# Kernel tuning notes

Hardware: AMD Instinct MI355X
Metric: run time of the kernel (lower is better)

Reference implementation:

```python
import jax, jax.numpy as jnp
import numpy as np

EXP_EMBD = 1024
EXP_Q_H = 8
EXP_HEAD_DIM = 256
EXP_KV_H = 1
EXP_KV_DIM = EXP_KV_H * EXP_HEAD_DIM  # 256
EXP_FFN = 4096
B, L, LC = 8, 512, 2048


def setup_inputs() -> dict:
    key = jax.random.key(0)
    ks = jax.random.split(key, 12)
    def w(k, shape):
        fan_in = shape[-1]
        return jax.random.normal(k, shape, jnp.float32) * (fan_in ** -0.5)
    return {
        "x": jax.random.normal(ks[0], (B, L, EXP_EMBD), jnp.float32),
        "text_k": jax.random.normal(ks[1], (B, LC, EXP_KV_DIM), jnp.float32),
        "text_v": jax.random.normal(ks[2], (B, LC, EXP_KV_DIM), jnp.float32),
        "ln1_w": jnp.ones((EXP_EMBD,), jnp.float32),
        "ln2_w": jnp.ones((EXP_EMBD,), jnp.float32),
        "Wq": w(ks[3], (EXP_Q_H * EXP_HEAD_DIM, EXP_EMBD)),
        "Wk": w(ks[4], (EXP_KV_DIM, EXP_KV_DIM)),
        "Wv": w(ks[5], (EXP_KV_DIM, EXP_KV_DIM)),
        "Wo": w(ks[6], (EXP_EMBD, EXP_Q_H * EXP_HEAD_DIM)),
        "Wg": w(ks[7], (EXP_FFN, EXP_EMBD)),
        "Wu": w(ks[8], (EXP_FFN, EXP_EMBD)),
        "Wd": w(ks[9], (EXP_EMBD, EXP_FFN)),
    }


def _rmsnorm(x, w):
    # torch.nn.RMSNorm with eps=None -> eps = finfo(dtype).eps
    eps = jnp.asarray(jnp.finfo(jnp.float32).eps, x.dtype)
    return x * jax.lax.rsqrt(jnp.mean(x * x, axis=-1, keepdims=True) + eps) * w


def _rope(x):
    # x: [B, L, H, D]
    b, l, h, d = x.shape
    d2 = d // 2
    ts = 10000.0 ** (2.0 / d * jnp.arange(d2, dtype=jnp.float32))  # [d2]
    rad = jnp.arange(l, dtype=jnp.float32)[:, None] / ts[None, :]  # [L, d2]
    s = jnp.sin(rad)[None, :, None, :]
    c = jnp.cos(rad)[None, :, None, :]
    x1, x2 = x[..., :d2], x[..., d2:]
    return jnp.concatenate([x1 * c - x2 * s, x2 * c + x1 * s], axis=-1)


def reference(x, text_k, text_v, ln1_w, ln2_w, Wq, Wk, Wv, Wo, Wg, Wu, Wd):
    b, l, _ = x.shape
    lc = text_k.shape[1]
    residual = x
    h = _rmsnorm(x, ln1_w)
    q = _rope((h @ Wq.T).reshape(b, l, EXP_Q_H, EXP_HEAD_DIM))          # [B,L,QH,D]
    k = (text_k @ Wk.T).reshape(b, lc, EXP_KV_H, EXP_HEAD_DIM)          # [B,Lc,KVH,D]
    v = (text_v @ Wv.T).reshape(b, lc, EXP_KV_H, EXP_HEAD_DIM)
    kv_map = (jnp.arange(EXP_Q_H) * EXP_KV_H) // EXP_Q_H                # GQA head map
    kh = jnp.take(k, kv_map, axis=2)                                    # [B,Lc,QH,D]
    vh = jnp.take(v, kv_map, axis=2)
    scale = 1.0 / np.sqrt(EXP_HEAD_DIM).astype(np.float32)
    scores = jnp.einsum('blhd,bchd->bhlc', q, kh) * scale               # [B,QH,L,Lc]
    attn = jax.nn.softmax(scores, axis=-1)
    ctx = jnp.einsum('bhlc,bchd->blhd', attn, vh).reshape(b, l, -1)
    x = ctx @ Wo.T + residual
    residual = x
    h = _rmsnorm(x, ln2_w)
    return (jax.nn.silu(h @ Wg.T) * (h @ Wu.T)) @ Wd.T + residual
```

## Files before the change

kernel.cpp:

```cpp
#include <hip/hip_runtime.h>

typedef __attribute__((ext_vector_type(4))) float f32x4;
typedef __attribute__((ext_vector_type(8))) short s16x8;
typedef __attribute__((ext_vector_type(4))) unsigned short u16x4;

#define B_    8
#define L_    512
#define LC_   2048
#define EMBD  1024

__device__ __forceinline__ float b2f(unsigned short u) {
  unsigned int i = ((unsigned int)u) << 16;
  float f; __builtin_memcpy(&f, &i, 4); return f;
}
__device__ __forceinline__ unsigned short f2b(float f) {
  unsigned int i; __builtin_memcpy(&i, &f, 4);
  unsigned int r = i + 0x7FFFu + ((i >> 16) & 1u);
  return (unsigned short)(r >> 16);
}

#define GLL16(g, l)                                                         \
  __builtin_amdgcn_global_load_lds(                                         \
      (__attribute__((address_space(1))) void*)(g),                         \
      (__attribute__((address_space(3))) void*)(l), 16, 0, 0)

#define VMCNT6() asm volatile("s_waitcnt vmcnt(6)" ::: "memory")
#define VMCNT0() asm volatile("s_waitcnt vmcnt(0)" ::: "memory")
#define LGKM0()  asm volatile("s_waitcnt lgkmcnt(0)" ::: "memory")

__global__ __launch_bounds__(256) void convert_f32_bf16(
    const float* __restrict__ in, unsigned short* __restrict__ out, int n4) {
  int i = blockIdx.x * 256 + threadIdx.x;
  if (i >= n4) return;
  float4 v = ((const float4*)in)[i];
  u16x4 o = { f2b(v.x), f2b(v.y), f2b(v.z), f2b(v.w) };
  ((u16x4*)out)[i] = o;
}

__global__ __launch_bounds__(256) void rmsnorm_kernel(
    const float* __restrict__ x, const float* __restrict__ w,
    unsigned short* __restrict__ out) {
  int row = blockIdx.x;
  int tid = threadIdx.x;
  float4 v = ((const float4*)(x + (size_t)row * EMBD))[tid];
  float ss = v.x*v.x + v.y*v.y + v.z*v.z + v.w*v.w;
#pragma unroll
  for (int o = 1; o < 64; o <<= 1) ss += __shfl_xor(ss, o);
  __shared__ float red[4];
  if ((tid & 63) == 0) red[tid >> 6] = ss;
  __syncthreads();
  float tot = red[0] + red[1] + red[2] + red[3];
  float rs = rsqrtf(tot * (1.0f / EMBD) + 1.1920928955078125e-07f);
  float4 wv = ((const float4*)w)[tid];
  u16x4 o = { f2b(v.x*rs*wv.x), f2b(v.y*rs*wv.y), f2b(v.z*rs*wv.z), f2b(v.w*rs*wv.w) };
  ((u16x4*)(out + (size_t)row * EMBD))[tid] = o;
}

__global__ __launch_bounds__(256) void rope_kernel(unsigned short* __restrict__ q) {
  int idx = blockIdx.x * 256 + threadIdx.x;
  int i   = idx & 127;
  int h   = (idx >> 7) & 7;
  int row = idx >> 10;
  int l   = row & (L_ - 1);
  size_t base = (size_t)row * 2048 + h * 256 + i;
  float x1 = b2f(q[base]);
  float x2 = b2f(q[base + 128]);
  float ts  = powf(10000.0f, (float)i * (2.0f / 256.0f));
  float rad = (float)l / ts;
  float s, c;
  sincosf(rad, &s, &c);
  q[base]       = f2b(x1 * c - x2 * s);
  q[base + 128] = f2b(x2 * c + x1 * s);
}

__global__ __launch_bounds__(256) void act_kernel(
    const unsigned short* __restrict__ g, const unsigned short* __restrict__ u,
    unsigned short* __restrict__ out, int n8) {
  int i = blockIdx.x * 256 + threadIdx.x;
  if (i >= n8) return;
  s16x8 gv = ((const s16x8*)g)[i];
  s16x8 uv = ((const s16x8*)u)[i];
  s16x8 ov;
#pragma unroll
  for (int j = 0; j < 8; ++j) {
    float gf = b2f((unsigned short)gv[j]);
    float uf = b2f((unsigned short)uv[j]);
    float s  = gf / (1.0f + __expf(-gf));
    ov[j] = (short)f2b(s * uf);
  }
  ((s16x8*)out)[i] = ov;
}

template <int ADD_RES, int OUT_BF16>
__global__ __launch_bounds__(256, 2) void gemm_nt(
    const unsigned short* __restrict__ A, const unsigned short* __restrict__ Bw,
    const float* __restrict__ Res, void* __restrict__ C, int M, int N, int K) {
  __shared__ unsigned short As[128 * 64];
  __shared__ unsigned short Bs[128 * 64];
  const int tid = threadIdx.x;
  const int lane = tid & 63, wid = tid >> 6;
  const int l15 = lane & 15, l4 = lane >> 4;
  const int wr = wid >> 1, wc = wid & 1;
  const int m0 = blockIdx.y * 128, n0 = blockIdx.x * 128;

  const f32x4 fz = {0.f, 0.f, 0.f, 0.f};
  f32x4 acc[4][4];
#pragma unroll
  for (int i = 0; i < 4; ++i)
#pragma unroll
    for (int j = 0; j < 4; ++j) acc[i][j] = fz;

  for (int k0 = 0; k0 < K; k0 += 64) {
    __syncthreads();
#pragma unroll
    for (int i = 0; i < 4; ++i) {
      int Li = i * 4096 + tid * 16;
      int row = Li >> 7;
      int kb = (Li & 127) ^ ((row & 7) << 4);
      GLL16((const char*)(A + (size_t)(m0 + row) * K + k0) + kb, (char*)As + Li);
      GLL16((const char*)(Bw + (size_t)(n0 + row) * K + k0) + kb, (char*)Bs + Li);
    }
    __syncthreads();
#pragma unroll
    for (int kk = 0; kk < 2; ++kk) {
      s16x8 af[4], bfr[4];
#pragma unroll
      for (int mi = 0; mi < 4; ++mi) {
        int row = wr * 64 + mi * 16 + l15;
        int kb = (kk * 64 + l4 * 16) ^ ((row & 7) << 4);
        af[mi] = *(const s16x8*)((const char*)As + row * 128 + kb);
      }
#pragma unroll
      for (int ni = 0; ni < 4; ++ni) {
        int row = wc * 64 + ni * 16 + l15;
        int kb = (kk * 64 + l4 * 16) ^ ((row & 7) << 4);
        bfr[ni] = *(const s16x8*)((const char*)Bs + row * 128 + kb);
      }
#pragma unroll
      for (int mi = 0; mi < 4; ++mi)
#pragma unroll
        for (int ni = 0; ni < 4; ++ni)
          acc[mi][ni] = __builtin_amdgcn_mfma_f32_16x16x32_bf16(
              af[mi], bfr[ni], acc[mi][ni], 0, 0, 0);
    }
  }
#pragma unroll
  for (int mi = 0; mi < 4; ++mi) {
#pragma unroll
    for (int r = 0; r < 4; ++r) {
      int grow = m0 + wr * 64 + mi * 16 + l4 * 4 + r;
      size_t base = (size_t)grow * N + n0 + wc * 64 + l15;
#pragma unroll
      for (int ni = 0; ni < 4; ++ni) {
        float v = acc[mi][ni][r];
        size_t idx = base + ni * 16;
        if (ADD_RES) v += Res[idx];
        if (OUT_BF16) ((unsigned short*)C)[idx] = f2b(v);
        else          ((float*)C)[idx] = v;
      }
    }
  }
}

__global__ __launch_bounds__(512, 2) void gemm256(
    const unsigned short* __restrict__ A, const unsigned short* __restrict__ Bw,
    unsigned short* __restrict__ C, int M, int N, int K) {
  extern __shared__ char smem[];
  const int tid = threadIdx.x;
  const int lane = tid & 63;
  const int wid = tid >> 6;
  const int wr = wid >> 2, wc = wid & 3;
  const int l15 = lane & 15, g = lane >> 4;
  int flat = blockIdx.y * 16 + blockIdx.x;
  flat = (flat & 7) * 32 + (flat >> 3);
  const int m0 = (flat >> 4) * 256, n0 = (flat & 15) * 256;
  const int T = K >> 6;
  const int swz = (l15 & 7) << 4;

  auto stage = [&](int t, int mat, int half) {
    char* dst = smem + mat * 65536 + (t & 1) * 32768 + half * 16384;
    const unsigned short* src = (mat ? Bw + (size_t)(n0 + half * 128) * K
                                     : A + (size_t)(m0 + half * 128) * K) + t * 64;
#pragma unroll
    for (int i = 0; i < 2; ++i) {
      int Li = i * 8192 + tid * 16;
      int row = Li >> 7;
      int kb = (Li & 127) ^ ((row & 7) << 4);
      GLL16((const char*)(src + (size_t)row * K) + kb, dst + Li);
    }
  };

  const f32x4 fz = {0.f, 0.f, 0.f, 0.f};
  f32x4 acc[2][2][4][2];
#pragma unroll
  for (int ms = 0; ms < 2; ++ms)
#pragma unroll
    for (int ns = 0; ns < 2; ++ns)
#pragma unroll
      for (int mi = 0; mi < 4; ++mi)
#pragma unroll
        for (int ni = 0; ni < 2; ++ni) acc[ms][ns][mi][ni] = fz;

  stage(0, 1, 0); stage(0, 1, 1); stage(0, 0, 0); stage(0, 0, 1);
  stage(1, 1, 0); stage(1, 1, 1); stage(1, 0, 0);
  VMCNT6();
  __builtin_amdgcn_s_barrier();

  for (int t = 0; t < T; ++t) {
    char* Ab = smem + (t & 1) * 32768 + wr * 16384;
    char* Bb = smem + 65536 + (t & 1) * 32768 + (wc >> 1) * 16384;
    const int bn = (wc & 1) * 64;
    s16x8 a[4][2], b0[2][2], b1[2][2];

#pragma unroll
    for (int mi = 0; mi < 4; ++mi) {
      int row = mi * 16 + l15;
#pragma unroll
      for (int kk = 0; kk < 2; ++kk)
        a[mi][kk] = *(const s16x8*)(Ab + row * 128 + ((kk * 64 + g * 16) ^ swz));
    }
#pragma unroll
    for (int ni = 0; ni < 2; ++ni) {
      int r0 = (bn + ni * 16 + l15) * 128;
      int r1 = (bn + 32 + ni * 16 + l15) * 128;
#pragma unroll
      for (int kk = 0; kk < 2; ++kk) {
        int ko = (kk * 64 + g * 16) ^ swz;
        b0[ni][kk] = *(const s16x8*)(Bb + r0 + ko);
        b1[ni][kk] = *(const s16x8*)(Bb + r1 + ko);
      }
    }
    if (t + 1 < T) stage(t + 1, 0, 1);
    __builtin_amdgcn_s_barrier();
    LGKM0();
    __builtin_amdgcn_sched_barrier(0);
    __builtin_amdgcn_s_setprio(1);
#pragma unroll
    for (int mi = 0; mi < 4; ++mi)
#pragma unroll
      for (int ni = 0; ni < 2; ++ni)
#pragma unroll
        for (int kk = 0; kk < 2; ++kk)
          acc[0][0][mi][ni] = __builtin_amdgcn_mfma_f32_16x16x32_bf16(
              a[mi][kk], b0[ni][kk], acc[0][0][mi][ni], 0, 0, 0);
    __builtin_amdgcn_s_setprio(0);
    __builtin_amdgcn_s_barrier();

    if (t + 2 < T) stage(t + 2, 1, 0);
    __builtin_amdgcn_s_barrier();
    __builtin_amdgcn_s_setprio(1);
#pragma unroll
    for (int mi = 0; mi < 4; ++mi)
#pragma unroll
      for (int ni = 0; ni < 2; ++ni)
#pragma unroll
        for (int kk = 0; kk < 2; ++kk)
          acc[0][1][mi][ni] = __builtin_amdgcn_mfma_f32_16x16x32_bf16(
              a[mi][kk], b1[ni][kk], acc[0][1][mi][ni], 0, 0, 0);
    __builtin_amdgcn_s_setprio(0);
    __builtin_amdgcn_s_barrier();

#pragma unroll
    for (int mi = 0; mi < 4; ++mi) {
      int row = 64 + mi * 16 + l15;
#pragma unroll
      for (int kk = 0; kk < 2; ++kk)
        a[mi][kk] = *(const s16x8*)(Ab + row * 128 + ((kk * 64 + g * 16) ^ swz));
    }
    if (t + 2 < T) stage(t + 2, 1, 1);
    __builtin_amdgcn_s_barrier();
    LGKM0();
    __builtin_amdgcn_sched_barrier(0);
    __builtin_amdgcn_s_setprio(1);
#pragma unroll
    for (int mi = 0; mi < 4; ++mi)
#pragma unroll
      for (int ni = 0; ni < 2; ++ni)
#pragma unroll
        for (int kk = 0; kk < 2; ++kk)
          acc[1][0][mi][ni] = __builtin_amdgcn_mfma_f32_16x16x32_bf16(
              a[mi][kk], b0[ni][kk], acc[1][0][mi][ni], 0, 0, 0);
    __builtin_amdgcn_s_setprio(0);
    __builtin_amdgcn_s_barrier();

    if (t + 2 < T) { stage(t + 2, 0, 0); VMCNT6(); }
    else           { VMCNT0(); }
    __builtin_amdgcn_s_barrier();
    __builtin_amdgcn_s_setprio(1);
#pragma unroll
    for (int mi = 0; mi < 4; ++mi)
#pragma unroll
      for (int ni = 0; ni < 2; ++ni)
#pragma unroll
        for (int kk = 0; kk < 2; ++kk)
          acc[1][1][mi][ni] = __builtin_amdgcn_mfma_f32_16x16x32_bf16(
              a[mi][kk], b1[ni][kk], acc[1][1][mi][ni], 0, 0, 0);
    __builtin_amdgcn_s_setprio(0);
    __builtin_amdgcn_s_barrier();
  }

#pragma unroll
  for (int ms = 0; ms < 2; ++ms)
#pragma unroll
    for (int mi = 0; mi < 4; ++mi)
#pragma unroll
      for (int r = 0; r < 4; ++r) {
        int grow = m0 + wr * 128 + ms * 64 + mi * 16 + g * 4 + r;
        size_t base = (size_t)grow * N + n0 + wc * 64;
#pragma unroll
        for (int ns = 0; ns < 2; ++ns)
#pragma unroll
          for (int ni = 0; ni < 2; ++ni)
            C[base + ns * 32 + ni * 16 + l15] = f2b(acc[ms][ns][mi][ni][r]);
      }
}

#define SWZV(d) (((((d) & 7) ^ (((d) >> 3) & 7))) << 4)

__global__ __launch_bounds__(512, 2) void attn_kernel(
    const unsigned short* __restrict__ Q,
    const unsigned short* __restrict__ Kc,
    const unsigned short* __restrict__ Vc,
    unsigned short* __restrict__ Ctx) {
  __shared__ unsigned short Ks[64 * 256];
  __shared__ unsigned short Vt[256 * 64];
  const int tid = threadIdx.x;
  const int lane = tid & 63, wid = tid >> 6;
  const int l15 = lane & 15, g = lane >> 4;
  const int qt = blockIdx.x, h = blockIdx.y, b = blockIdx.z;

  const size_t qrow = (size_t)(b * L_ + qt * 128 + wid * 16 + l15);
  const unsigned short* qp = Q + qrow * 2048 + h * 256;
  s16x8 qf[8];
#pragma unroll
  for (int kc = 0; kc < 8; ++kc) qf[kc] = *(const s16x8*)(qp + kc * 32 + g * 8);

  const f32x4 fz = {0.f, 0.f, 0.f, 0.f};
  f32x4 oacc[16];
#pragma unroll
  for (int i = 0; i < 16; ++i) oacc[i] = fz;
  float m_run = -__builtin_inff(), l_run = 0.f;

  const unsigned short* Kb = Kc + (size_t)b * LC_ * 256;
  const unsigned short* Vb = Vc + (size_t)b * LC_ * 256;

  for (int kt = 0; kt < LC_ / 64; ++kt) {
    __syncthreads();
#pragma unroll
    for (int i = 0; i < 4; ++i) {
      int Li = i * 8192 + tid * 16;
      int row = Li >> 9;
      int kb = (Li & 511) ^ ((row & 7) << 4);
      GLL16((const char*)(Kb + (size_t)(kt * 64 + row) * 256) + kb, (char*)Ks + Li);
    }
#pragma unroll
    for (int p = 0; p < 2; ++p) {
      int id = p * 512 + tid;
      int dgrp = id & 31;
      int kvp = id >> 5;
      int d0 = dgrp * 8, kv0 = kvp * 2;
      const unsigned short* v0p = Vb + (size_t)(kt * 64 + kv0) * 256 + d0;
      s16x8 r0 = *(const s16x8*)v0p;
      s16x8 r1 = *(const s16x8*)(v0p + 256);
#pragma unroll
      for (int j = 0; j < 8; ++j) {
        int d = d0 + j;
        unsigned int val = (unsigned int)(unsigned short)r0[j] |
                           ((unsigned int)(unsigned short)r1[j] << 16);
        *(unsigned int*)((char*)Vt + d * 128 + ((kv0 * 2) ^ SWZV(d))) = val;
      }
    }
    __syncthreads();

    f32x4 sacc[4];
#pragma unroll
    for (int mi = 0; mi < 4; ++mi) sacc[mi] = fz;
#pragma unroll
    for (int mi = 0; mi < 4; ++mi) {
      int row = mi * 16 + l15;
      int swz = (row & 7) << 4;
#pragma unroll
      for (int kc = 0; kc < 8; ++kc) {
        s16x8 kf = *(const s16x8*)((const char*)Ks + row * 512 + ((kc * 64 + g * 16) ^ swz));
        sacc[mi] = __builtin_amdgcn_mfma_f32_16x16x32_bf16(kf, qf[kc], sacc[mi], 0, 0, 0);
      }
    }
    float sv[4][4];
    float mt = -__builtin_inff();
#pragma unroll
    for (int mi = 0; mi < 4; ++mi)
#pragma unroll
      for (int r = 0; r < 4; ++r) {
        float t = sacc[mi][r] * 0.0625f;
        sv[mi][r] = t;
        mt = fmaxf(mt, t);
      }
    mt = fmaxf(mt, __shfl_xor(mt, 16));
    mt = fmaxf(mt, __shfl_xor(mt, 32));
    float mnew = fmaxf(m_run, mt);
    float alpha = __expf(m_run - mnew);
    float rs = 0.f;
#pragma unroll
    for (int mi = 0; mi < 4; ++mi)
#pragma unroll
      for (int r = 0; r < 4; ++r) {
        float p = __expf(sv[mi][r] - mnew);
        sv[mi][r] = p;
        rs += p;
      }
    rs += __shfl_xor(rs, 16);
    rs += __shfl_xor(rs, 32);
    l_run = l_run * alpha + rs;
    m_run = mnew;
    float af4[4];
#pragma unroll
    for (int r = 0; r < 4; ++r) af4[r] = __shfl(alpha, g * 4 + r);
#pragma unroll
    for (int nd = 0; nd < 16; ++nd)
#pragma unroll
      for (int r = 0; r < 4; ++r) oacc[nd][r] *= af4[r];
    unsigned int pk[4][2];
#pragma unroll
    for (int ni = 0; ni < 4; ++ni) {
      pk[ni][0] = (unsigned int)f2b(sv[ni][0]) | ((unsigned int)f2b(sv[ni][1]) << 16);
      pk[ni][1] = (unsigned int)f2b(sv[ni][2]) | ((unsigned int)f2b(sv[ni][3]) << 16);
    }
    int cbase = (g & 1) << 3;
#pragma unroll
    for (int t = 0; t < 2; ++t) {
      unsigned int w[4];
#pragma unroll
      for (int jj = 0; jj < 4; ++jj) {
        int c = cbase + (jj << 1);
        int src = ((c >> 2) << 4) + l15;
        unsigned int ra = __shfl(pk[2 * t][jj & 1], src);
        unsigned int rb = __shfl(pk[2 * t + 1][jj & 1], src);
        w[jj] = (g < 2) ? ra : rb;
      }
      union { unsigned int u[4]; s16x8 v; } cvt;
      cvt.u[0] = w[0]; cvt.u[1] = w[1]; cvt.u[2] = w[2]; cvt.u[3] = w[3];
      s16x8 ap = cvt.v;
#pragma unroll
      for (int nd = 0; nd < 16; ++nd) {
        int d = nd * 16 + l15;
        s16x8 vf = *(const s16x8*)((const char*)Vt + d * 128 + ((t * 64 + g * 16) ^ SWZV(d)));
        oacc[nd] = __builtin_amdgcn_mfma_f32_16x16x32_bf16(ap, vf, oacc[nd], 0, 0, 0);
      }
    }
  }
  float lf[4];
#pragma unroll
  for (int r = 0; r < 4; ++r) lf[r] = 1.0f / __shfl(l_run, g * 4 + r);
  const size_t orow0 = (size_t)(b * L_ + qt * 128 + wid * 16);
#pragma unroll
  for (int r = 0; r < 4; ++r) {
    size_t base = (orow0 + g * 4 + r) * 2048 + h * 256 + l15;
#pragma unroll
    for (int nd = 0; nd < 16; ++nd)
      Ctx[base + nd * 16] = f2b(oacc[nd][r] * lf[r]);
  }
}

extern "C" void kernel_launch(void* const* d_in, const int* in_sizes, int n_in,
                              void* d_out, int out_size, void* d_ws, size_t ws_size,
                              hipStream_t stream) {
  const float* x   = (const float*)d_in[0];
  const float* tk  = (const float*)d_in[1];
  const float* tv  = (const float*)d_in[2];
  const float* ln1 = (const float*)d_in[3];
  const float* ln2 = (const float*)d_in[4];
  const float* Wq  = (const float*)d_in[5];
  const float* Wk  = (const float*)d_in[6];
  const float* Wv  = (const float*)d_in[7];
  const float* Wo  = (const float*)d_in[8];
  const float* Wg  = (const float*)d_in[9];
  const float* Wu  = (const float*)d_in[10];
  const float* Wd  = (const float*)d_in[11];
  float* out = (float*)d_out;
  char* ws = (char*)d_ws;

  (void)hipFuncSetAttribute((const void*)gemm256,
                            hipFuncAttributeMaxDynamicSharedMemorySize, 131072);

  unsigned short* tk_bf  = (unsigned short*)(ws + 0);
  unsigned short* tv_bf  = (unsigned short*)(ws + 8388608);
  unsigned short* k_bf   = (unsigned short*)(ws + 16777216);
  unsigned short* v_bf   = (unsigned short*)(ws + 25165824);
  unsigned short* g_bf   = (unsigned short*)(ws + 0);
  unsigned short* q_bf   = (unsigned short*)(ws + 33554432);
  unsigned short* ctx_bf = (unsigned short*)(ws + 50331648);
  unsigned short* u_bf   = (unsigned short*)(ws + 33554432);
  unsigned short* wq_bf  = (unsigned short*)(ws + 67108864);
  unsigned short* wk_bf  = (unsigned short*)(ws + 71303168);
  unsigned short* wv_bf  = (unsigned short*)(ws + 71434240);
  unsigned short* wo_bf  = (unsigned short*)(ws + 71565312);
  unsigned short* wg_bf  = (unsigned short*)(ws + 75759616);
  unsigned short* wu_bf  = (unsigned short*)(ws + 84148224);
  unsigned short* wd_bf  = (unsigned short*)(ws + 92536832);
  unsigned short* h_bf   = (unsigned short*)(ws + 100925440);
  float*          x2     = (float*)(ws + 109314048);

  dim3 blk(256);
  auto cvt = [&](const float* src, unsigned short* dst, int n) {
    convert_f32_bf16<<<dim3(n / 1024), blk, 0, stream>>>(src, dst, n / 4);
  };
  cvt(Wq, wq_bf, 2097152);
  cvt(Wk, wk_bf, 65536);
  cvt(Wv, wv_bf, 65536);
  cvt(Wo, wo_bf, 2097152);
  cvt(Wg, wg_bf, 4194304);
  cvt(Wu, wu_bf, 4194304);
  cvt(Wd, wd_bf, 4194304);
  cvt(tk, tk_bf, 4194304);
  cvt(tv, tv_bf, 4194304);

  rmsnorm_kernel<<<dim3(4096), blk, 0, stream>>>(x, ln1, h_bf);
  gemm_nt<0, 1><<<dim3(16, 32), blk, 0, stream>>>(h_bf, wq_bf, nullptr, q_bf, 4096, 2048, 1024);
  rope_kernel<<<dim3(16384), blk, 0, stream>>>(q_bf);
  gemm_nt<0, 1><<<dim3(2, 128), blk, 0, stream>>>(tk_bf, wk_bf, nullptr, k_bf, 16384, 256, 256);
  gemm_nt<0, 1><<<dim3(2, 128), blk, 0, stream>>>(tv_bf, wv_bf, nullptr, v_bf, 16384, 256, 256);
  attn_kernel<<<dim3(4, 8, 8), dim3(512), 0, stream>>>(q_bf, k_bf, v_bf, ctx_bf);
  gemm_nt<1, 0><<<dim3(8, 32), blk, 0, stream>>>(ctx_bf, wo_bf, x, x2, 4096, 1024, 2048);
  rmsnorm_kernel<<<dim3(4096), blk, 0, stream>>>(x2, ln2, h_bf);
  gemm256<<<dim3(16, 16), dim3(512), 131072, stream>>>(h_bf, wg_bf, g_bf, 4096, 4096, 1024);
  gemm256<<<dim3(16, 16), dim3(512), 131072, stream>>>(h_bf, wu_bf, u_bf, 4096, 4096, 1024);
  act_kernel<<<dim3(8192), blk, 0, stream>>>(g_bf, u_bf, g_bf, 2097152);
  gemm_nt<1, 0><<<dim3(8, 32), blk, 0, stream>>>(g_bf, wd_bf, x2, out, 4096, 1024, 4096);
}
```

Measured before the change: 435.2 us.

## Double-buffer K/V tiles in attention with warp-specialized prefetch and packed V transpose

The attention kernel now keeps two LDS buffers each for K and transposed V, 128KB of dynamic shared memory in total. Half the threads issue async K loads for the next tile while the other half load V into registers, and the compute of the current tile overlaps these loads. The V transpose now builds full 16-byte LDS writes with byte-permute instructions instead of many 4-byte stores, using a simpler swizzle. The cost is occupancy: launch bounds drop from 2 blocks per CU to 1, and the V stores still happen after compute, behind a wait and a barrier.

```diff
diff --git a/kernel.cpp b/kernel.cpp
--- a/kernel.cpp
+++ b/kernel.cpp
@@ -315,15 +315,12 @@
       }
 }
 
-#define SWZV(d) (((((d) & 7) ^ (((d) >> 3) & 7))) << 4)
-
-__global__ __launch_bounds__(512, 2) void attn_kernel(
+__global__ __launch_bounds__(512, 1) void attn_kernel(
     const unsigned short* __restrict__ Q,
     const unsigned short* __restrict__ Kc,
     const unsigned short* __restrict__ Vc,
     unsigned short* __restrict__ Ctx) {
-  __shared__ unsigned short Ks[64 * 256];
-  __shared__ unsigned short Vt[256 * 64];
+  extern __shared__ char ats[];
   const int tid = threadIdx.x;
   const int lane = tid & 63, wid = tid >> 6;
   const int l15 = lane & 15, g = lane >> 4;
@@ -344,33 +341,55 @@
   const unsigned short* Kb = Kc + (size_t)b * LC_ * 256;
   const unsigned short* Vb = Vc + (size_t)b * LC_ * 256;
 
-  for (int kt = 0; kt < LC_ / 64; ++kt) {
-    __syncthreads();
-#pragma unroll
-    for (int i = 0; i < 4; ++i) {
-      int Li = i * 8192 + tid * 16;
+  const int vtid = tid & 255;
+  const int dgrp = vtid & 31, kvoct = vtid >> 5;
+  const int vslot = (kvoct ^ (dgrp & 7)) << 4;
+  s16x8 vr[8];
+
+  auto stageK = [&](int kt1, char* dstK) {
+#pragma unroll
+    for (int i = 0; i < 8; ++i) {
+      int Li = i * 4096 + tid * 16;
       int row = Li >> 9;
       int kb = (Li & 511) ^ ((row & 7) << 4);
-      GLL16((const char*)(Kb + (size_t)(kt * 64 + row) * 256) + kb, (char*)Ks + Li);
-    }
-#pragma unroll
-    for (int p = 0; p < 2; ++p) {
-      int id = p * 512 + tid;
-      int dgrp = id & 31;
-      int kvp = id >> 5;
-      int d0 = dgrp * 8, kv0 = kvp * 2;
-      const unsigned short* v0p = Vb + (size_t)(kt * 64 + kv0) * 256 + d0;
-      s16x8 r0 = *(const s16x8*)v0p;
-      s16x8 r1 = *(const s16x8*)(v0p + 256);
-#pragma unroll
-      for (int j = 0; j < 8; ++j) {
-        int d = d0 + j;
-        unsigned int val = (unsigned int)(unsigned short)r0[j] |
-                           ((unsigned int)(unsigned short)r1[j] << 16);
-        *(unsigned int*)((char*)Vt + d * 128 + ((kv0 * 2) ^ SWZV(d))) = val;
-      }
-    }
-    __syncthreads();
+      GLL16((const char*)(Kb + (size_t)(kt1 * 64 + row) * 256) + kb, dstK + Li);
+    }
+  };
+  auto loadV = [&](int kt1) {
+    const unsigned short* vp = Vb + (size_t)(kt1 * 64 + kvoct * 8) * 256 + dgrp * 8;
+#pragma unroll
+    for (int i = 0; i < 8; ++i) vr[i] = *(const s16x8*)(vp + i * 256);
+  };
+  auto writeV = [&](char* dstV) {
+#pragma unroll
+    for (int j = 0; j < 8; ++j) {
+      union { unsigned u[4]; s16x8 v; } w;
+#pragma unroll
+      for (int k2 = 0; k2 < 4; ++k2) {
+        unsigned bl = ((const unsigned*)&vr[2 * k2])[j >> 1];
+        unsigned ah = ((const unsigned*)&vr[2 * k2 + 1])[j >> 1];
+        w.u[k2] = __builtin_amdgcn_perm(ah, bl, (j & 1) ? 0x07060302u : 0x05040100u);
+      }
+      *(s16x8*)(dstV + (dgrp * 8 + j) * 128 + vslot) = w.v;
+    }
+  };
+
+  if (tid < 256) stageK(0, ats);
+  else           loadV(0);
+  if (tid >= 256) { VMCNT0(); writeV(ats + 65536); }
+  VMCNT0();
+  __syncthreads();
+
+  for (int kt = 0; kt < LC_ / 64; ++kt) {
+    char* KsB = ats + (kt & 1) * 32768;
+    char* VtB = ats + 65536 + (kt & 1) * 32768;
+    char* KsN = ats + ((kt + 1) & 1) * 32768;
+    char* VtN = ats + 65536 + ((kt + 1) & 1) * 32768;
+    const bool more = (kt + 1 < LC_ / 64);
+    if (more) {
+      if (tid < 256) stageK(kt + 1, KsN);
+      else           loadV(kt + 1);
+    }
 
     f32x4 sacc[4];
 #pragma unroll
@@ -381,7 +400,7 @@
       int swz = (row & 7) << 4;
 #pragma unroll
       for (int kc = 0; kc < 8; ++kc) {
-        s16x8 kf = *(const s16x8*)((const char*)Ks + row * 512 + ((kc * 64 + g * 16) ^ swz));
+        s16x8 kf = *(const s16x8*)(KsB + row * 512 + ((kc * 64 + g * 16) ^ swz));
         sacc[mi] = __builtin_amdgcn_mfma_f32_16x16x32_bf16(kf, qf[kc], sacc[mi], 0, 0, 0);
       }
     }
@@ -427,14 +446,14 @@
     }
     int cbase = (g & 1) << 3;
 #pragma unroll
-    for (int t = 0; t < 2; ++t) {
+    for (int tt = 0; tt < 2; ++tt) {
       unsigned int w[4];
 #pragma unroll
       for (int jj = 0; jj < 4; ++jj) {
         int c = cbase + (jj << 1);
         int src = ((c >> 2) << 4) + l15;
-        unsigned int ra = __shfl(pk[2 * t][jj & 1], src);
-        unsigned int rb = __shfl(pk[2 * t + 1][jj & 1], src);
+        unsigned int ra = __shfl(pk[2 * tt][jj & 1], src);
+        unsigned int rb = __shfl(pk[2 * tt + 1][jj & 1], src);
         w[jj] = (g < 2) ? ra : rb;
       }
       union { unsigned int u[4]; s16x8 v; } cvt;
@@ -443,10 +462,15 @@
 #pragma unroll
       for (int nd = 0; nd < 16; ++nd) {
         int d = nd * 16 + l15;
-        s16x8 vf = *(const s16x8*)((const char*)Vt + d * 128 + ((t * 64 + g * 16) ^ SWZV(d)));
+        s16x8 vf = *(const s16x8*)(VtB + d * 128 +
+                                   ((tt * 64 + g * 16) ^ (((d >> 3) & 7) << 4)));
         oacc[nd] = __builtin_amdgcn_mfma_f32_16x16x32_bf16(ap, vf, oacc[nd], 0, 0, 0);
       }
     }
+
+    if (more && tid >= 256) { VMCNT0(); writeV(VtN); }
+    VMCNT0();
+    __syncthreads();
   }
   float lf[4];
 #pragma unroll
@@ -481,6 +505,8 @@
 
   (void)hipFuncSetAttribute((const void*)gemm256,
                             hipFuncAttributeMaxDynamicSharedMemorySize, 131072);
+  (void)hipFuncSetAttribute((const void*)attn_kernel,
+                            hipFuncAttributeMaxDynamicSharedMemorySize, 131072);
 
   unsigned short* tk_bf  = (unsigned short*)(ws + 0);
   unsigned short* tv_bf  = (unsigned short*)(ws + 8388608);
@@ -519,7 +545,7 @@
   rope_kernel<<<dim3(16384), blk, 0, stream>>>(q_bf);
   gemm_nt<0, 1><<<dim3(2, 128), blk, 0, stream>>>(tk_bf, wk_bf, nullptr, k_bf, 16384, 256, 256);
   gemm_nt<0, 1><<<dim3(2, 128), blk, 0, stream>>>(tv_bf, wv_bf, nullptr, v_bf, 16384, 256, 256);
-  attn_kernel<<<dim3(4, 8, 8), dim3(512), 0, stream>>>(q_bf, k_bf, v_bf, ctx_bf);
+  attn_kernel<<<dim3(4, 8, 8), dim3(512), 131072, stream>>>(q_bf, k_bf, v_bf, ctx_bf);
   gemm_nt<1, 0><<<dim3(8, 32), blk, 0, stream>>>(ctx_bf, wo_bf, x, x2, 4096, 1024, 2048);
   rmsnorm_kernel<<<dim3(4096), blk, 0, stream>>>(x2, ln2, h_bf);
   gemm256<<<dim3(16, 16), dim3(512), 131072, stream>>>(h_bf, wg_bf, g_bf, 4096, 4096, 1024);
```

New measurement: 448.7 us. 3.1% more time.
